# Kernel tuning notes

Hardware: AMD Instinct MI355X
Metric: run time of the kernel (lower is better)

Reference implementation:

```python
import jax, jax.numpy as jnp
import numpy as np

B, N, M, D = 4, 256, 256, 524
EPS = 1e-8


def setup_inputs() -> dict:
    key = jax.random.key(0)
    ks = jax.random.split(key, 16)

    def lin(k, fin, fout):
        kw, kb = jax.random.split(k)
        w = jax.random.normal(kw, (fin, fout), jnp.float32) * (1.0 / np.sqrt(fin))
        b = jax.random.normal(kb, (fout,), jnp.float32) * 0.01
        return w, b

    cw1, cb1 = lin(ks[3], D, 256)
    cw2, cb2 = lin(ks[4], 256, 128)
    cw3, cb3 = lin(ks[5], 128, 1)
    ow1, ob1 = lin(ks[6], D, 128)
    ow2, ob2 = lin(ks[7], 128, 1)
    return {
        "L_bat": jax.random.normal(ks[0], (B, N, M, D), jnp.float32),
        "src_centroids": jax.random.normal(ks[1], (B, N, 3), jnp.float32),
        "tgt_centroids": jax.random.normal(ks[2], (B, M, 3), jnp.float32),
        "cw1": cw1, "cb1": cb1, "cw2": cw2, "cb2": cb2, "cw3": cw3, "cb3": cb3,
        "ow1": ow1, "ob1": ob1, "ow2": ow2, "ob2": ob2,
    }


def _rot_mat_to_quat(R):
    # Shepperd's method, fully batched, scalar-last [x, y, z, w].
    tr = R[:, 0, 0] + R[:, 1, 1] + R[:, 2, 2]
    s0 = jnp.sqrt(jnp.maximum(tr + 1.0, 1e-10)) * 2
    q0 = jnp.stack([(R[:, 2, 1] - R[:, 1, 2]) / s0, (R[:, 0, 2] - R[:, 2, 0]) / s0,
                    (R[:, 1, 0] - R[:, 0, 1]) / s0, 0.25 * s0], axis=-1)
    s1 = jnp.sqrt(jnp.maximum(1.0 + R[:, 0, 0] - R[:, 1, 1] - R[:, 2, 2], 1e-10)) * 2
    q1 = jnp.stack([0.25 * s1, (R[:, 0, 1] + R[:, 1, 0]) / s1,
                    (R[:, 0, 2] + R[:, 2, 0]) / s1, (R[:, 2, 1] - R[:, 1, 2]) / s1], axis=-1)
    s2 = jnp.sqrt(jnp.maximum(1.0 + R[:, 1, 1] - R[:, 0, 0] - R[:, 2, 2], 1e-10)) * 2
    q2 = jnp.stack([(R[:, 0, 1] + R[:, 1, 0]) / s2, 0.25 * s2,
                    (R[:, 1, 2] + R[:, 2, 1]) / s2, (R[:, 0, 2] - R[:, 2, 0]) / s2], axis=-1)
    s3 = jnp.sqrt(jnp.maximum(1.0 + R[:, 2, 2] - R[:, 0, 0] - R[:, 1, 1], 1e-10)) * 2
    q3 = jnp.stack([(R[:, 0, 2] + R[:, 2, 0]) / s3, (R[:, 1, 2] + R[:, 2, 1]) / s3,
                    0.25 * s3, (R[:, 1, 0] - R[:, 0, 1]) / s3], axis=-1)
    c1 = (tr > 0)[:, None]
    c2 = ((R[:, 0, 0] > R[:, 1, 1]) & (R[:, 0, 0] > R[:, 2, 2]))[:, None]
    c3 = (R[:, 1, 1] > R[:, 2, 2])[:, None]
    q = jnp.where(c1, q0, jnp.where(c2, q1, jnp.where(c3, q2, q3)))
    return q / jnp.maximum(jnp.linalg.norm(q, axis=-1, keepdims=True), 1e-12)


def _forward(L_bat, src_centroids, tgt_centroids,
             cw1, cb1, cw2, cb2, cw3, cb3, ow1, ob1, ow2, ob2):
    # corr MLP: [B,N,M,D] -> [B,N,M]
    h = jax.nn.relu(L_bat @ cw1 + cb1)
    h = jax.nn.relu(h @ cw2 + cb2)
    corr_scores = (h @ cw3 + cb3)[..., 0]
    corr_weights = jax.nn.softmax(corr_scores, axis=2)              # softmax over M
    matched = jnp.einsum('bnmd,bnm->bnd', L_bat, corr_weights)      # [B,N,D]
    overlap = jax.nn.sigmoid(jax.nn.relu(matched @ ow1 + ob1) @ ow2 + ob2)  # [B,N,1]
    tgt_matched = jnp.einsum('bnm,bmc->bnc', corr_weights, tgt_centroids)   # [B,N,3]
    w = overlap[..., 0]
    w_norm = w / jnp.maximum(w.sum(axis=1, keepdims=True), EPS)
    src_bar = jnp.einsum('bn,bnc->bc', w_norm, src_centroids)
    tgt_bar = jnp.einsum('bn,bnc->bc', w_norm, tgt_matched)
    src_c = src_centroids - src_bar[:, None, :]
    tgt_c = tgt_matched - tgt_bar[:, None, :]
    H = jnp.einsum('bnc,bn,bnd->bcd', src_c, w_norm, tgt_c)          # [B,3,3]
    U, S, Vh = jnp.linalg.svd(H)
    R_raw = jnp.einsum('bki,bjk->bij', Vh, U)                        # Vh^T @ U^T
    det_sign = jnp.sign(jnp.linalg.det(R_raw))
    corr_fix = jnp.stack([jnp.ones_like(det_sign), jnp.ones_like(det_sign), det_sign], axis=-1)
    Vh_fix = Vh * corr_fix[:, :, None]
    R = jnp.einsum('bki,bjk->bij', Vh_fix, U)
    translation = tgt_bar - jnp.einsum('bij,bj->bi', R, src_bar)
    quaternion = _rot_mat_to_quat(R)
    return quaternion, translation, R, corr_weights, overlap


def reference(L_bat, src_centroids, tgt_centroids,
              cw1, cb1, cw2, cb2, cw3, cb3, ow1, ob1, ow2, ob2):
    return _forward(L_bat, src_centroids, tgt_centroids,
                    cw1, cb1, cw2, cb2, cw3, cb3, ow1, ob1, ow2, ob2)
```

## Files before the change

### kernel.cpp

```cpp
#include <hip/hip_runtime.h>
#include <hip/hip_bf16.h>


#define D_ 524
#define CW_OFF 64
#define OV_OFF 262208

typedef __attribute__((ext_vector_type(8))) short short8;
typedef __attribute__((ext_vector_type(4))) float floatx4;

__device__ __forceinline__ short f2bf(float v) {
  unsigned u = __builtin_bit_cast(unsigned, v);
  unsigned r = (u + 0x7FFFu + ((u >> 16) & 1u)) >> 16;
  return (short)(unsigned short)r;
}
__device__ __forceinline__ float bf2f(short s) {
  unsigned u = ((unsigned)(unsigned short)s) << 16;
  return __builtin_bit_cast(float, u);
}

__global__ void prep_kernel(const float* __restrict__ cw1, const float* __restrict__ cw2,
                            short* __restrict__ w1h, short* __restrict__ w1l,
                            short* __restrict__ w2h, short* __restrict__ w2l) {
  int t = blockIdx.x * 256 + threadIdx.x;
  if (t < 17408) {
    int lane = t & 63, ct = (t >> 6) & 15, kk = t >> 10;
    int col = ct * 16 + (lane & 15);
    int kbase = kk * 32 + ((lane >> 4) << 3);
#pragma unroll
    for (int i = 0; i < 8; ++i) {
      int k = kbase + i;
      float v = (k < D_) ? cw1[k * 256 + col] : 0.f;
      short h = f2bf(v);
      w1h[t * 8 + i] = h;
      w1l[t * 8 + i] = f2bf(v - bf2f(h));
    }
  } else if (t < 21504) {
    int u = t - 17408;
    int lane = u & 63, ct = (u >> 6) & 7, kk = u >> 9;
    int col = ct * 16 + (lane & 15);
    int kbase = kk * 32 + ((lane >> 4) << 3);
#pragma unroll
    for (int i = 0; i < 8; ++i) {
      int k = kbase + i;
      float v = cw2[k * 128 + col];
      short h = f2bf(v);
      w2h[u * 8 + i] = h;
      w2l[u * 8 + i] = f2bf(v - bf2f(h));
    }
  }
}

__global__ __launch_bounds__(256, 2) void main_kernel(
    const float* __restrict__ L, const float* __restrict__ tgt,
    const float* __restrict__ cb1, const float* __restrict__ cb2,
    const float* __restrict__ cw3, const float* __restrict__ cb3,
    const float* __restrict__ ow1, const float* __restrict__ ob1,
    const float* __restrict__ ow2, const float* __restrict__ ob2,
    const short8* __restrict__ w1h, const short8* __restrict__ w1l,
    const short8* __restrict__ w2h, const short8* __restrict__ w2l,
    float* __restrict__ out, float* __restrict__ tgtm) {
  int bn = blockIdx.x;
  int b = bn >> 8;
  int t = threadIdx.x;
  int w = t >> 6, lane = t & 63, l15 = lane & 15, q = lane >> 4;

  __shared__ __attribute__((aligned(16))) short Ah[2][64 * 40];
  __shared__ __attribute__((aligned(16))) short h1s[64 * 264];
  __shared__ float p_all[256];
  __shared__ float redw[256];
  __shared__ float m_s[524];
  __shared__ float o1s[128];
  __shared__ float sS;

  const float* Lbn = L + (size_t)bn * (256 * D_);
  float mac0 = 0.f, mac1 = 0.f, mac2 = 0.f;

  int srow = t >> 2, sko = (t & 3) * 8;

#pragma unroll 1
  for (int mt = 0; mt < 4; ++mt) {
    int m0 = mt * 64;
    const float* Lrow = Lbn + (size_t)(m0 + srow) * D_;

    floatx4 acc[4][4];
#pragma unroll
    for (int r = 0; r < 4; ++r)
#pragma unroll
      for (int c = 0; c < 4; ++c) acc[r][c] = (floatx4)(0.f);

    {
      floatx4 v0 = *(const floatx4*)(Lrow + sko);
      floatx4 v1 = *(const floatx4*)(Lrow + sko + 4);
      short8 sv;
#pragma unroll
      for (int j = 0; j < 4; ++j) { sv[j] = f2bf(v0[j]); sv[4 + j] = f2bf(v1[j]); }
      *(short8*)&Ah[0][srow * 40 + sko] = sv;
    }
    __syncthreads();

#pragma unroll 1
    for (int kk = 0; kk < 17; ++kk) {
      int cb = kk & 1;
      floatx4 nv0, nv1;
      if (kk < 15) {
        nv0 = *(const floatx4*)(Lrow + (kk + 1) * 32 + sko);
        nv1 = *(const floatx4*)(Lrow + (kk + 1) * 32 + sko + 4);
      } else if (kk == 15) {
#pragma unroll
        for (int j = 0; j < 4; ++j) {
          int k0 = 512 + sko + j, k1 = 512 + sko + 4 + j;
          nv0[j] = (k0 < D_) ? Lrow[k0] : 0.f;
          nv1[j] = (k1 < D_) ? Lrow[k1] : 0.f;
        }
      }
      short8 bh[4], bl[4];
#pragma unroll
      for (int c = 0; c < 4; ++c) {
        int f = (kk * 16 + (w * 4 + c)) * 64 + lane;
        bh[c] = w1h[f];
        bl[c] = w1l[f];
      }
      short8 af[4];
#pragma unroll
      for (int r = 0; r < 4; ++r)
        af[r] = *(const short8*)&Ah[cb][(r * 16 + l15) * 40 + q * 8];
#pragma unroll
      for (int r = 0; r < 4; ++r)
#pragma unroll
        for (int c = 0; c < 4; ++c) {
          acc[r][c] = __builtin_amdgcn_mfma_f32_16x16x32_bf16(af[r], bh[c], acc[r][c], 0, 0, 0);
          acc[r][c] = __builtin_amdgcn_mfma_f32_16x16x32_bf16(af[r], bl[c], acc[r][c], 0, 0, 0);
        }
      if (kk < 16) {
        short8 sv;
#pragma unroll
        for (int j = 0; j < 4; ++j) { sv[j] = f2bf(nv0[j]); sv[4 + j] = f2bf(nv1[j]); }
        *(short8*)&Ah[cb ^ 1][srow * 40 + sko] = sv;
      }
      __syncthreads();
    }

#pragma unroll
    for (int c = 0; c < 4; ++c) {
      int col = (w * 4 + c) * 16 + l15;
      float b1 = cb1[col];
#pragma unroll
      for (int r = 0; r < 4; ++r)
#pragma unroll
        for (int i = 0; i < 4; ++i) {
          int row = r * 16 + q * 4 + i;
          h1s[row * 264 + col] = f2bf(fmaxf(acc[r][c][i] + b1, 0.f));
        }
    }
    __syncthreads();

    floatx4 ac2[4][2];
#pragma unroll
    for (int r = 0; r < 4; ++r)
#pragma unroll
      for (int c = 0; c < 2; ++c) ac2[r][c] = (floatx4)(0.f);
#pragma unroll 1
    for (int kk = 0; kk < 8; ++kk) {
      short8 a2[4];
#pragma unroll
      for (int r = 0; r < 4; ++r)
        a2[r] = *(const short8*)&h1s[(r * 16 + l15) * 264 + kk * 32 + q * 8];
      short8 b2h_[2], b2l_[2];
#pragma unroll
      for (int c = 0; c < 2; ++c) {
        int f = (kk * 8 + (w * 2 + c)) * 64 + lane;
        b2h_[c] = w2h[f];
        b2l_[c] = w2l[f];
      }
#pragma unroll
      for (int r = 0; r < 4; ++r)
#pragma unroll
        for (int c = 0; c < 2; ++c) {
          ac2[r][c] = __builtin_amdgcn_mfma_f32_16x16x32_bf16(a2[r], b2h_[c], ac2[r][c], 0, 0, 0);
          ac2[r][c] = __builtin_amdgcn_mfma_f32_16x16x32_bf16(a2[r], b2l_[c], ac2[r][c], 0, 0, 0);
        }
    }

    float pr[4][4];
#pragma unroll
    for (int r = 0; r < 4; ++r)
#pragma unroll
      for (int i = 0; i < 4; ++i) pr[r][i] = 0.f;
#pragma unroll
    for (int c = 0; c < 2; ++c) {
      int col = (w * 2 + c) * 16 + l15;
      float b2 = cb2[col], w3 = cw3[col];
#pragma unroll
      for (int r = 0; r < 4; ++r)
#pragma unroll
        for (int i = 0; i < 4; ++i)
          pr[r][i] += fmaxf(ac2[r][c][i] + b2, 0.f) * w3;
    }
#pragma unroll
    for (int m = 1; m <= 8; m <<= 1)
#pragma unroll
      for (int r = 0; r < 4; ++r)
#pragma unroll
        for (int i = 0; i < 4; ++i) pr[r][i] += __shfl_xor(pr[r][i], m, 64);
    if (l15 == 0) {
#pragma unroll
      for (int r = 0; r < 4; ++r)
#pragma unroll
        for (int i = 0; i < 4; ++i) redw[w * 64 + r * 16 + q * 4 + i] = pr[r][i];
    }
    __syncthreads();
    if (t < 64) {
      float s = redw[t] + redw[64 + t] + redw[128 + t] + redw[192 + t] + cb3[0];
      p_all[m0 + t] = expf(s);
    }
    __syncthreads();

#pragma unroll 4
    for (int m = 0; m < 64; ++m) {
      float pm = p_all[m0 + m];
      const float* Lr = Lbn + (size_t)(m0 + m) * D_;
      mac0 += pm * Lr[t];
      mac1 += pm * Lr[t + 256];
      if (t < 12) mac2 += pm * Lr[t + 512];
    }
  }

  if (t < 64) redw[t] = p_all[t] + p_all[t + 64] + p_all[t + 128] + p_all[t + 192];
  __syncthreads();
  if (t == 0) {
    float s = 0.f;
    for (int i = 0; i < 64; ++i) s += redw[i];
    sS = 1.f / s;
  }
  __syncthreads();
  float invS = sS;
  out[CW_OFF + bn * 256 + t] = p_all[t] * invS;
  m_s[t] = mac0 * invS;
  m_s[t + 256] = mac1 * invS;
  if (t < 12) m_s[t + 512] = mac2 * invS;
  __syncthreads();

  if (t < 128) {
    float a = ob1[t];
#pragma unroll 4
    for (int d = 0; d < D_; ++d) a += m_s[d] * ow1[d * 128 + t];
    o1s[t] = fmaxf(a, 0.f) * ow2[t];
  }
  if (t < 96) {
    int c = t % 3, g = t / 3;
    float s = 0.f;
#pragma unroll
    for (int m = 0; m < 8; ++m) s += p_all[g * 8 + m] * tgt[((b * 256) + g * 8 + m) * 3 + c];
    redw[t] = s;
  }
  __syncthreads();
  if (t == 0) {
    float a = ob2[0];
    for (int j = 0; j < 128; ++j) a += o1s[j];
    out[OV_OFF + bn] = 1.f / (1.f + expf(-a));
  }
  if (t < 3) {
    float s = 0.f;
    for (int g = 0; g < 32; ++g) s += redw[g * 3 + t];
    tgtm[bn * 3 + t] = s * invS;
  }
}

__global__ __launch_bounds__(256) void finalize_kernel(const float* __restrict__ src,
                                                       const float* __restrict__ tgtm,
                                                       float* __restrict__ out) {
  int b = blockIdx.x, t = threadIdx.x;
  __shared__ float red[256];

  auto bsum = [&](float v) -> float {
    red[t] = v;
    __syncthreads();
    for (int s = 128; s > 0; s >>= 1) {
      if (t < s) red[t] += red[t + s];
      __syncthreads();
    }
    float r = red[0];
    __syncthreads();
    return r;
  };

  float wv = out[OV_OFF + b * 256 + t];
  float Sw = bsum(wv);
  float wn = wv / fmaxf(Sw, 1e-8f);
  float sc[3], tm[3];
#pragma unroll
  for (int c = 0; c < 3; ++c) {
    sc[c] = src[(b * 256 + t) * 3 + c];
    tm[c] = tgtm[(b * 256 + t) * 3 + c];
  }
  float sb[3], tb[3];
#pragma unroll
  for (int c = 0; c < 3; ++c) sb[c] = bsum(wn * sc[c]);
#pragma unroll
  for (int c = 0; c < 3; ++c) tb[c] = bsum(wn * tm[c]);
  float Hv[9];
#pragma unroll
  for (int c = 0; c < 3; ++c)
#pragma unroll
    for (int d = 0; d < 3; ++d)
      Hv[c * 3 + d] = bsum((sc[c] - sb[c]) * wn * (tm[d] - tb[d]));

  if (t == 0) {
    double H[3][3];
    for (int i = 0; i < 3; ++i)
      for (int j = 0; j < 3; ++j) H[i][j] = (double)Hv[i * 3 + j];
    double A[3][3], V[3][3] = {{1, 0, 0}, {0, 1, 0}, {0, 0, 1}};
    for (int i = 0; i < 3; ++i)
      for (int j = 0; j < 3; ++j) {
        double s = 0;
        for (int k = 0; k < 3; ++k) s += H[k][i] * H[k][j];
        A[i][j] = s;
      }
    const int PQ[3][2] = {{0, 1}, {0, 2}, {1, 2}};
    for (int sweep = 0; sweep < 30; ++sweep)
      for (int r = 0; r < 3; ++r) {
        int p = PQ[r][0], qq = PQ[r][1];
        double apq = A[p][qq];
        if (fabs(apq) < 1e-300) continue;
        double tau = (A[qq][qq] - A[p][p]) / (2.0 * apq);
        double tt = (tau >= 0 ? 1.0 : -1.0) / (fabs(tau) + sqrt(1.0 + tau * tau));
        double cc = 1.0 / sqrt(1.0 + tt * tt), ss = tt * cc;
        for (int k = 0; k < 3; ++k) {
          double akp = A[k][p], akq = A[k][qq];
          A[k][p] = cc * akp - ss * akq;
          A[k][qq] = ss * akp + cc * akq;
        }
        for (int k = 0; k < 3; ++k) {
          double apk = A[p][k], aqk = A[qq][k];
          A[p][k] = cc * apk - ss * aqk;
          A[qq][k] = ss * apk + cc * aqk;
        }
        for (int k = 0; k < 3; ++k) {
          double vkp = V[k][p], vkq = V[k][qq];
          V[k][p] = cc * vkp - ss * vkq;
          V[k][qq] = ss * vkp + cc * vkq;
        }
      }
    int idx[3] = {0, 1, 2};
    for (int i = 0; i < 2; ++i)
      for (int j = i + 1; j < 3; ++j)
        if (A[idx[j]][idx[j]] > A[idx[i]][idx[i]]) { int tmp = idx[i]; idx[i] = idx[j]; idx[j] = tmp; }
    double v0[3], v1[3], v2[3];
    for (int k = 0; k < 3; ++k) {
      v0[k] = V[k][idx[0]];
      v1[k] = V[k][idx[1]];
      v2[k] = V[k][idx[2]];
    }
    double u0[3], u1[3], u2[3];
    for (int j = 0; j < 3; ++j) {
      u0[j] = H[j][0] * v0[0] + H[j][1] * v0[1] + H[j][2] * v0[2];
      u1[j] = H[j][0] * v1[0] + H[j][1] * v1[1] + H[j][2] * v1[2];
    }
    double n0 = sqrt(u0[0] * u0[0] + u0[1] * u0[1] + u0[2] * u0[2]);
    n0 = (n0 > 1e-300) ? n0 : 1e-300;
    for (int j = 0; j < 3; ++j) u0[j] /= n0;
    double d01 = u0[0] * u1[0] + u0[1] * u1[1] + u0[2] * u1[2];
    for (int j = 0; j < 3; ++j) u1[j] -= d01 * u0[j];
    double n1 = sqrt(u1[0] * u1[0] + u1[1] * u1[1] + u1[2] * u1[2]);
    n1 = (n1 > 1e-300) ? n1 : 1e-300;
    for (int j = 0; j < 3; ++j) u1[j] /= n1;
    u2[0] = u0[1] * u1[2] - u0[2] * u1[1];
    u2[1] = u0[2] * u1[0] - u0[0] * u1[2];
    u2[2] = u0[0] * u1[1] - u0[1] * u1[0];
    double Rr[3][3];
    for (int i = 0; i < 3; ++i)
      for (int j = 0; j < 3; ++j)
        Rr[i][j] = v0[i] * u0[j] + v1[i] * u1[j] + v2[i] * u2[j];
    double det = Rr[0][0] * (Rr[1][1] * Rr[2][2] - Rr[1][2] * Rr[2][1]) -
                 Rr[0][1] * (Rr[1][0] * Rr[2][2] - Rr[1][2] * Rr[2][0]) +
                 Rr[0][2] * (Rr[1][0] * Rr[2][1] - Rr[1][1] * Rr[2][0]);
    double sg = (det >= 0) ? 1.0 : -1.0;
    double R[3][3];
    for (int i = 0; i < 3; ++i)
      for (int j = 0; j < 3; ++j)
        R[i][j] = v0[i] * u0[j] + v1[i] * u1[j] + sg * v2[i] * u2[j];
    double trv[3];
    for (int i = 0; i < 3; ++i)
      trv[i] = (double)tb[i] - (R[i][0] * sb[0] + R[i][1] * sb[1] + R[i][2] * sb[2]);
    double qv[4];
    double tr = R[0][0] + R[1][1] + R[2][2];
    if (tr > 0) {
      double S = sqrt(fmax(tr + 1.0, 1e-10)) * 2.0;
      qv[0] = (R[2][1] - R[1][2]) / S;
      qv[1] = (R[0][2] - R[2][0]) / S;
      qv[2] = (R[1][0] - R[0][1]) / S;
      qv[3] = 0.25 * S;
    } else if (R[0][0] > R[1][1] && R[0][0] > R[2][2]) {
      double S = sqrt(fmax(1.0 + R[0][0] - R[1][1] - R[2][2], 1e-10)) * 2.0;
      qv[0] = 0.25 * S;
      qv[1] = (R[0][1] + R[1][0]) / S;
      qv[2] = (R[0][2] + R[2][0]) / S;
      qv[3] = (R[2][1] - R[1][2]) / S;
    } else if (R[1][1] > R[2][2]) {
      double S = sqrt(fmax(1.0 + R[1][1] - R[0][0] - R[2][2], 1e-10)) * 2.0;
      qv[0] = (R[0][1] + R[1][0]) / S;
      qv[1] = 0.25 * S;
      qv[2] = (R[1][2] + R[2][1]) / S;
      qv[3] = (R[0][2] - R[2][0]) / S;
    } else {
      double S = sqrt(fmax(1.0 + R[2][2] - R[0][0] - R[1][1], 1e-10)) * 2.0;
      qv[0] = (R[0][2] + R[2][0]) / S;
      qv[1] = (R[1][2] + R[2][1]) / S;
      qv[2] = 0.25 * S;
      qv[3] = (R[1][0] - R[0][1]) / S;
    }
    double qn = sqrt(qv[0] * qv[0] + qv[1] * qv[1] + qv[2] * qv[2] + qv[3] * qv[3]);
    qn = fmax(qn, 1e-12);
    for (int k = 0; k < 4; ++k) out[b * 4 + k] = (float)(qv[k] / qn);
    for (int i = 0; i < 3; ++i) out[16 + b * 3 + i] = (float)trv[i];
    for (int i = 0; i < 3; ++i)
      for (int j = 0; j < 3; ++j) out[28 + b * 9 + i * 3 + j] = (float)R[i][j];
  }
}

extern "C" void kernel_launch(void* const* d_in, const int* in_sizes, int n_in,
                              void* d_out, int out_size, void* d_ws, size_t ws_size,
                              hipStream_t stream) {
  const float* L = (const float*)d_in[0];
  const float* src = (const float*)d_in[1];
  const float* tgt = (const float*)d_in[2];
  const float* cw1 = (const float*)d_in[3];
  const float* cb1 = (const float*)d_in[4];
  const float* cw2 = (const float*)d_in[5];
  const float* cb2 = (const float*)d_in[6];
  const float* cw3 = (const float*)d_in[7];
  const float* cb3 = (const float*)d_in[8];
  const float* ow1 = (const float*)d_in[9];
  const float* ob1 = (const float*)d_in[10];
  const float* ow2 = (const float*)d_in[11];
  const float* ob2 = (const float*)d_in[12];
  float* out = (float*)d_out;

  char* ws = (char*)d_ws;
  short* w1h = (short*)(ws);
  short* w1l = (short*)(ws + 278528);
  short* w2h = (short*)(ws + 557056);
  short* w2l = (short*)(ws + 622592);
  float* tgtm = (float*)(ws + 688128);

  hipLaunchKernelGGL(prep_kernel, dim3(84), dim3(256), 0, stream, cw1, cw2, w1h, w1l, w2h, w2l);
  hipLaunchKernelGGL(main_kernel, dim3(1024), dim3(256), 0, stream,
                     L, tgt, cb1, cb2, cw3, cb3, ow1, ob1, ow2, ob2,
                     (const short8*)w1h, (const short8*)w1l,
                     (const short8*)w2h, (const short8*)w2l, out, tgtm);
  hipLaunchKernelGGL(finalize_kernel, dim3(4), dim3(256), 0, stream, src, tgtm, out);
}
```

Before: 1.140 ms.

## Fold overlap MLP first layer into GEMM via linearity, widen block to 512 threads

Uses linearity to replace the weighted sum of L rows followed by the ow1 matvec with an extra GEMM column block (ow1 appended to cw1 in bf16 hi only), accumulated per row and then weighted by p. This removes the second full pass over L from global memory for the weighted mean. The block doubles to 512 threads processing two 64-row tiles per k-step, and the padding of the second-layer buffer changes. The change adds MFMA work and drops precision on the ow1 path to single bf16, which risks accuracy.

```diff
diff --git a/kernel.cpp b/kernel.cpp
--- a/kernel.cpp
+++ b/kernel.cpp
@@ -5,6 +5,12 @@
 #define D_ 524
 #define CW_OFF 64
 #define OV_OFF 262208
+
+#define W1H_OFF 0
+#define W1L_OFF 417792
+#define W2H_OFF 696320
+#define W2L_OFF 761856
+#define TGTM_OFF 827392
 
 typedef __attribute__((ext_vector_type(8))) short short8;
 typedef __attribute__((ext_vector_type(4))) float floatx4;
@@ -19,31 +25,32 @@
   return __builtin_bit_cast(float, u);
 }
 
-__global__ void prep_kernel(const float* __restrict__ cw1, const float* __restrict__ cw2,
+__global__ void prep_kernel(const float* __restrict__ cw1, const float* __restrict__ ow1,
+                            const float* __restrict__ cw2,
                             short* __restrict__ w1h, short* __restrict__ w1l,
                             short* __restrict__ w2h, short* __restrict__ w2l) {
   int t = blockIdx.x * 256 + threadIdx.x;
-  if (t < 17408) {
-    int lane = t & 63, ct = (t >> 6) & 15, kk = t >> 10;
-    int col = ct * 16 + (lane & 15);
-    int kbase = kk * 32 + ((lane >> 4) << 3);
+  if (t < 26112) {
+    int lane = t & 63, ct = (t >> 6) % 24, kk = t / 1536;
+    int cl = lane & 15, kb = kk * 32 + ((lane >> 4) << 3);
+    bool isW1 = ct < 16;
+    int lo_base = ((kk * 16 + ct) * 64 + lane) * 8;
 #pragma unroll
     for (int i = 0; i < 8; ++i) {
-      int k = kbase + i;
-      float v = (k < D_) ? cw1[k * 256 + col] : 0.f;
+      int k = kb + i;
+      float v = 0.f;
+      if (k < D_) v = isW1 ? cw1[k * 256 + ct * 16 + cl] : ow1[k * 128 + (ct - 16) * 16 + cl];
       short h = f2bf(v);
       w1h[t * 8 + i] = h;
-      w1l[t * 8 + i] = f2bf(v - bf2f(h));
-    }
-  } else if (t < 21504) {
-    int u = t - 17408;
+      if (isW1) w1l[lo_base + i] = f2bf(v - bf2f(h));
+    }
+  } else if (t < 30208) {
+    int u = t - 26112;
     int lane = u & 63, ct = (u >> 6) & 7, kk = u >> 9;
-    int col = ct * 16 + (lane & 15);
-    int kbase = kk * 32 + ((lane >> 4) << 3);
+    int col = ct * 16 + (lane & 15), kb = kk * 32 + ((lane >> 4) << 3);
 #pragma unroll
     for (int i = 0; i < 8; ++i) {
-      int k = kbase + i;
-      float v = cw2[k * 128 + col];
+      float v = cw2[(kb + i) * 128 + col];
       short h = f2bf(v);
       w2h[u * 8 + i] = h;
       w2l[u * 8 + i] = f2bf(v - bf2f(h));
@@ -51,51 +58,51 @@
   }
 }
 
-__global__ __launch_bounds__(256, 2) void main_kernel(
+__global__ __launch_bounds__(512, 2) void main_kernel(
     const float* __restrict__ L, const float* __restrict__ tgt,
     const float* __restrict__ cb1, const float* __restrict__ cb2,
     const float* __restrict__ cw3, const float* __restrict__ cb3,
-    const float* __restrict__ ow1, const float* __restrict__ ob1,
-    const float* __restrict__ ow2, const float* __restrict__ ob2,
+    const float* __restrict__ ob1, const float* __restrict__ ow2,
+    const float* __restrict__ ob2,
     const short8* __restrict__ w1h, const short8* __restrict__ w1l,
     const short8* __restrict__ w2h, const short8* __restrict__ w2l,
     float* __restrict__ out, float* __restrict__ tgtm) {
-  int bn = blockIdx.x;
-  int b = bn >> 8;
-  int t = threadIdx.x;
+  int bn = blockIdx.x, b = bn >> 8, t = threadIdx.x;
   int w = t >> 6, lane = t & 63, l15 = lane & 15, q = lane >> 4;
 
-  __shared__ __attribute__((aligned(16))) short Ah[2][64 * 40];
-  __shared__ __attribute__((aligned(16))) short h1s[64 * 264];
+  __shared__ __attribute__((aligned(16))) short Ah[2][2][64 * 40];
+  __shared__ __attribute__((aligned(16))) short h1s[64 * 272];
   __shared__ float p_all[256];
-  __shared__ float redw[256];
-  __shared__ float m_s[524];
-  __shared__ float o1s[128];
+  __shared__ float redw[512];
   __shared__ float sS;
 
   const float* Lbn = L + (size_t)bn * (256 * D_);
-  float mac0 = 0.f, mac1 = 0.f, mac2 = 0.f;
-
-  int srow = t >> 2, sko = (t & 3) * 8;
+  float ua = 0.f;
+
+  int mt_s = t >> 8, srow = (t >> 2) & 63, sko = (t & 3) * 8;
 
 #pragma unroll 1
-  for (int mt = 0; mt < 4; ++mt) {
-    int m0 = mt * 64;
-    const float* Lrow = Lbn + (size_t)(m0 + srow) * D_;
-
-    floatx4 acc[4][4];
-#pragma unroll
-    for (int r = 0; r < 4; ++r)
-#pragma unroll
-      for (int c = 0; c < 4; ++c) acc[r][c] = (floatx4)(0.f);
+  for (int mp = 0; mp < 2; ++mp) {
+    const float* Lr0 = Lbn + (size_t)(mp * 128 + mt_s * 64 + srow) * D_;
+
+    floatx4 acc[2][4][2];
+    floatx4 accg[2][4];
+#pragma unroll
+    for (int mt = 0; mt < 2; ++mt)
+#pragma unroll
+      for (int r = 0; r < 4; ++r) {
+        acc[mt][r][0] = (floatx4)(0.f);
+        acc[mt][r][1] = (floatx4)(0.f);
+        accg[mt][r] = (floatx4)(0.f);
+      }
 
     {
-      floatx4 v0 = *(const floatx4*)(Lrow + sko);
-      floatx4 v1 = *(const floatx4*)(Lrow + sko + 4);
+      floatx4 v0 = *(const floatx4*)(Lr0 + sko);
+      floatx4 v1 = *(const floatx4*)(Lr0 + sko + 4);
       short8 sv;
 #pragma unroll
       for (int j = 0; j < 4; ++j) { sv[j] = f2bf(v0[j]); sv[4 + j] = f2bf(v1[j]); }
-      *(short8*)&Ah[0][srow * 40 + sko] = sv;
+      *(short8*)&Ah[0][mt_s][srow * 40 + sko] = sv;
     }
     __syncthreads();
 
@@ -104,125 +111,115 @@
       int cb = kk & 1;
       floatx4 nv0, nv1;
       if (kk < 15) {
-        nv0 = *(const floatx4*)(Lrow + (kk + 1) * 32 + sko);
-        nv1 = *(const floatx4*)(Lrow + (kk + 1) * 32 + sko + 4);
+        nv0 = *(const floatx4*)(Lr0 + (kk + 1) * 32 + sko);
+        nv1 = *(const floatx4*)(Lr0 + (kk + 1) * 32 + sko + 4);
       } else if (kk == 15) {
 #pragma unroll
         for (int j = 0; j < 4; ++j) {
-          int k0 = 512 + sko + j, k1 = 512 + sko + 4 + j;
-          nv0[j] = (k0 < D_) ? Lrow[k0] : 0.f;
-          nv1[j] = (k1 < D_) ? Lrow[k1] : 0.f;
-        }
-      }
-      short8 bh[4], bl[4];
-#pragma unroll
-      for (int c = 0; c < 4; ++c) {
-        int f = (kk * 16 + (w * 4 + c)) * 64 + lane;
-        bh[c] = w1h[f];
-        bl[c] = w1l[f];
-      }
-      short8 af[4];
-#pragma unroll
-      for (int r = 0; r < 4; ++r)
-        af[r] = *(const short8*)&Ah[cb][(r * 16 + l15) * 40 + q * 8];
-#pragma unroll
-      for (int r = 0; r < 4; ++r)
-#pragma unroll
-        for (int c = 0; c < 4; ++c) {
-          acc[r][c] = __builtin_amdgcn_mfma_f32_16x16x32_bf16(af[r], bh[c], acc[r][c], 0, 0, 0);
-          acc[r][c] = __builtin_amdgcn_mfma_f32_16x16x32_bf16(af[r], bl[c], acc[r][c], 0, 0, 0);
+          int k0 = 512 + sko + j, k1 = 516 + sko + j;
+          nv0[j] = (k0 < D_) ? Lr0[k0] : 0.f;
+          nv1[j] = (k1 < D_) ? Lr0[k1] : 0.f;
+        }
+      }
+      short8 bh0 = w1h[(kk * 24 + 2 * w) * 64 + lane];
+      short8 bh1 = w1h[(kk * 24 + 2 * w + 1) * 64 + lane];
+      short8 gh = w1h[(kk * 24 + 16 + w) * 64 + lane];
+      short8 bl0 = w1l[(kk * 16 + 2 * w) * 64 + lane];
+      short8 bl1 = w1l[(kk * 16 + 2 * w + 1) * 64 + lane];
+      short8 af[2][4];
+#pragma unroll
+      for (int mt = 0; mt < 2; ++mt)
+#pragma unroll
+        for (int r = 0; r < 4; ++r)
+          af[mt][r] = *(const short8*)&Ah[cb][mt][(r * 16 + l15) * 40 + q * 8];
+#pragma unroll
+      for (int mt = 0; mt < 2; ++mt)
+#pragma unroll
+        for (int r = 0; r < 4; ++r) {
+          acc[mt][r][0] = __builtin_amdgcn_mfma_f32_16x16x32_bf16(af[mt][r], bh0, acc[mt][r][0], 0, 0, 0);
+          acc[mt][r][0] = __builtin_amdgcn_mfma_f32_16x16x32_bf16(af[mt][r], bl0, acc[mt][r][0], 0, 0, 0);
+          acc[mt][r][1] = __builtin_amdgcn_mfma_f32_16x16x32_bf16(af[mt][r], bh1, acc[mt][r][1], 0, 0, 0);
+          acc[mt][r][1] = __builtin_amdgcn_mfma_f32_16x16x32_bf16(af[mt][r], bl1, acc[mt][r][1], 0, 0, 0);
+          accg[mt][r] = __builtin_amdgcn_mfma_f32_16x16x32_bf16(af[mt][r], gh, accg[mt][r], 0, 0, 0);
         }
       if (kk < 16) {
         short8 sv;
 #pragma unroll
         for (int j = 0; j < 4; ++j) { sv[j] = f2bf(nv0[j]); sv[4 + j] = f2bf(nv1[j]); }
-        *(short8*)&Ah[cb ^ 1][srow * 40 + sko] = sv;
+        *(short8*)&Ah[cb ^ 1][mt_s][srow * 40 + sko] = sv;
       }
       __syncthreads();
     }
 
-#pragma unroll
-    for (int c = 0; c < 4; ++c) {
-      int col = (w * 4 + c) * 16 + l15;
-      float b1 = cb1[col];
+#pragma unroll 1
+    for (int mt = 0; mt < 2; ++mt) {
+      int m0 = mp * 128 + mt * 64;
+#pragma unroll
+      for (int c = 0; c < 2; ++c) {
+        int col = (2 * w + c) * 16 + l15;
+        float b1 = cb1[col];
+#pragma unroll
+        for (int r = 0; r < 4; ++r)
+#pragma unroll
+          for (int i = 0; i < 4; ++i)
+            h1s[(r * 16 + q * 4 + i) * 272 + col] = f2bf(fmaxf(acc[mt][r][c][i] + b1, 0.f));
+      }
+      __syncthreads();
+
+      floatx4 ac2[4];
+#pragma unroll
+      for (int r = 0; r < 4; ++r) ac2[r] = (floatx4)(0.f);
+#pragma unroll 1
+      for (int kk = 0; kk < 8; ++kk) {
+        short8 b2h_ = w2h[(kk * 8 + w) * 64 + lane];
+        short8 b2l_ = w2l[(kk * 8 + w) * 64 + lane];
+        short8 a2[4];
+#pragma unroll
+        for (int r = 0; r < 4; ++r)
+          a2[r] = *(const short8*)&h1s[(r * 16 + l15) * 272 + kk * 32 + q * 8];
+#pragma unroll
+        for (int r = 0; r < 4; ++r) {
+          ac2[r] = __builtin_amdgcn_mfma_f32_16x16x32_bf16(a2[r], b2h_, ac2[r], 0, 0, 0);
+          ac2[r] = __builtin_amdgcn_mfma_f32_16x16x32_bf16(a2[r], b2l_, ac2[r], 0, 0, 0);
+        }
+      }
+      int col2 = w * 16 + l15;
+      float b2 = cb2[col2], w3 = cw3[col2];
+      float pr[4][4];
 #pragma unroll
       for (int r = 0; r < 4; ++r)
 #pragma unroll
-        for (int i = 0; i < 4; ++i) {
-          int row = r * 16 + q * 4 + i;
-          h1s[row * 264 + col] = f2bf(fmaxf(acc[r][c][i] + b1, 0.f));
-        }
-    }
-    __syncthreads();
-
-    floatx4 ac2[4][2];
-#pragma unroll
-    for (int r = 0; r < 4; ++r)
-#pragma unroll
-      for (int c = 0; c < 2; ++c) ac2[r][c] = (floatx4)(0.f);
-#pragma unroll 1
-    for (int kk = 0; kk < 8; ++kk) {
-      short8 a2[4];
+        for (int i = 0; i < 4; ++i)
+          pr[r][i] = fmaxf(ac2[r][i] + b2, 0.f) * w3;
+#pragma unroll
+      for (int m = 1; m <= 8; m <<= 1)
+#pragma unroll
+        for (int r = 0; r < 4; ++r)
+#pragma unroll
+          for (int i = 0; i < 4; ++i) pr[r][i] += __shfl_xor(pr[r][i], m, 64);
+      if (l15 == 0) {
+#pragma unroll
+        for (int r = 0; r < 4; ++r)
+#pragma unroll
+          for (int i = 0; i < 4; ++i) redw[w * 64 + r * 16 + q * 4 + i] = pr[r][i];
+      }
+      __syncthreads();
+      if (t < 64) {
+        float s = cb3[0];
+#pragma unroll
+        for (int ww = 0; ww < 8; ++ww) s += redw[ww * 64 + t];
+        p_all[m0 + t] = expf(s);
+      }
+      __syncthreads();
+      float gv = 0.f;
 #pragma unroll
       for (int r = 0; r < 4; ++r)
-        a2[r] = *(const short8*)&h1s[(r * 16 + l15) * 264 + kk * 32 + q * 8];
-      short8 b2h_[2], b2l_[2];
-#pragma unroll
-      for (int c = 0; c < 2; ++c) {
-        int f = (kk * 8 + (w * 2 + c)) * 64 + lane;
-        b2h_[c] = w2h[f];
-        b2l_[c] = w2l[f];
-      }
-#pragma unroll
-      for (int r = 0; r < 4; ++r)
-#pragma unroll
-        for (int c = 0; c < 2; ++c) {
-          ac2[r][c] = __builtin_amdgcn_mfma_f32_16x16x32_bf16(a2[r], b2h_[c], ac2[r][c], 0, 0, 0);
-          ac2[r][c] = __builtin_amdgcn_mfma_f32_16x16x32_bf16(a2[r], b2l_[c], ac2[r][c], 0, 0, 0);
-        }
-    }
-
-    float pr[4][4];
-#pragma unroll
-    for (int r = 0; r < 4; ++r)
-#pragma unroll
-      for (int i = 0; i < 4; ++i) pr[r][i] = 0.f;
-#pragma unroll
-    for (int c = 0; c < 2; ++c) {
-      int col = (w * 2 + c) * 16 + l15;
-      float b2 = cb2[col], w3 = cw3[col];
-#pragma unroll
-      for (int r = 0; r < 4; ++r)
 #pragma unroll
         for (int i = 0; i < 4; ++i)
-          pr[r][i] += fmaxf(ac2[r][c][i] + b2, 0.f) * w3;
-    }
-#pragma unroll
-    for (int m = 1; m <= 8; m <<= 1)
-#pragma unroll
-      for (int r = 0; r < 4; ++r)
-#pragma unroll
-        for (int i = 0; i < 4; ++i) pr[r][i] += __shfl_xor(pr[r][i], m, 64);
-    if (l15 == 0) {
-#pragma unroll
-      for (int r = 0; r < 4; ++r)
-#pragma unroll
-        for (int i = 0; i < 4; ++i) redw[w * 64 + r * 16 + q * 4 + i] = pr[r][i];
-    }
-    __syncthreads();
-    if (t < 64) {
-      float s = redw[t] + redw[64 + t] + redw[128 + t] + redw[192 + t] + cb3[0];
-      p_all[m0 + t] = expf(s);
-    }
-    __syncthreads();
-
-#pragma unroll 4
-    for (int m = 0; m < 64; ++m) {
-      float pm = p_all[m0 + m];
-      const float* Lr = Lbn + (size_t)(m0 + m) * D_;
-      mac0 += pm * Lr[t];
-      mac1 += pm * Lr[t + 256];
-      if (t < 12) mac2 += pm * Lr[t + 512];
+          gv += p_all[m0 + r * 16 + q * 4 + i] * accg[mt][r][i];
+      gv += __shfl_xor(gv, 16, 64);
+      gv += __shfl_xor(gv, 32, 64);
+      ua += gv;
     }
   }
 
@@ -235,34 +232,32 @@
   }
   __syncthreads();
   float invS = sS;
-  out[CW_OFF + bn * 256 + t] = p_all[t] * invS;
-  m_s[t] = mac0 * invS;
-  m_s[t + 256] = mac1 * invS;
-  if (t < 12) m_s[t + 512] = mac2 * invS;
-  __syncthreads();
-
-  if (t < 128) {
-    float a = ob1[t];
-#pragma unroll 4
-    for (int d = 0; d < D_; ++d) a += m_s[d] * ow1[d * 128 + t];
-    o1s[t] = fmaxf(a, 0.f) * ow2[t];
+  if (t < 256) out[CW_OFF + bn * 256 + t] = p_all[t] * invS;
+
+  {
+    float u = ua * invS + ob1[w * 16 + l15];
+    float r = fmaxf(u, 0.f) * ow2[w * 16 + l15];
+    if (q != 0) r = 0.f;
+#pragma unroll
+    for (int m = 1; m <= 32; m <<= 1) r += __shfl_xor(r, m, 64);
+    if (lane == 0) redw[256 + w] = r;
   }
   if (t < 96) {
     int c = t % 3, g = t / 3;
     float s = 0.f;
 #pragma unroll
     for (int m = 0; m < 8; ++m) s += p_all[g * 8 + m] * tgt[((b * 256) + g * 8 + m) * 3 + c];
-    redw[t] = s;
+    redw[320 + t] = s;
   }
   __syncthreads();
   if (t == 0) {
-    float a = ob2[0];
-    for (int j = 0; j < 128; ++j) a += o1s[j];
-    out[OV_OFF + bn] = 1.f / (1.f + expf(-a));
+    float o = ob2[0];
+    for (int ww = 0; ww < 8; ++ww) o += redw[256 + ww];
+    out[OV_OFF + bn] = 1.f / (1.f + expf(-o));
   }
   if (t < 3) {
     float s = 0.f;
-    for (int g = 0; g < 32; ++g) s += redw[g * 3 + t];
+    for (int g = 0; g < 32; ++g) s += redw[320 + g * 3 + t];
     tgtm[bn * 3 + t] = s * invS;
   }
 }
@@ -438,15 +433,15 @@
   float* out = (float*)d_out;
 
   char* ws = (char*)d_ws;
-  short* w1h = (short*)(ws);
-  short* w1l = (short*)(ws + 278528);
-  short* w2h = (short*)(ws + 557056);
-  short* w2l = (short*)(ws + 622592);
-  float* tgtm = (float*)(ws + 688128);
-
-  hipLaunchKernelGGL(prep_kernel, dim3(84), dim3(256), 0, stream, cw1, cw2, w1h, w1l, w2h, w2l);
-  hipLaunchKernelGGL(main_kernel, dim3(1024), dim3(256), 0, stream,
-                     L, tgt, cb1, cb2, cw3, cb3, ow1, ob1, ow2, ob2,
+  short* w1h = (short*)(ws + W1H_OFF);
+  short* w1l = (short*)(ws + W1L_OFF);
+  short* w2h = (short*)(ws + W2H_OFF);
+  short* w2l = (short*)(ws + W2L_OFF);
+  float* tgtm = (float*)(ws + TGTM_OFF);
+
+  hipLaunchKernelGGL(prep_kernel, dim3(118), dim3(256), 0, stream, cw1, ow1, cw2, w1h, w1l, w2h, w2l);
+  hipLaunchKernelGGL(main_kernel, dim3(1024), dim3(512), 0, stream,
+                     L, tgt, cb1, cb2, cw3, cb3, ob1, ow2, ob2,
                      (const short8*)w1h, (const short8*)w1l,
                      (const short8*)w2h, (const short8*)w2l, out, tgtm);
   hipLaunchKernelGGL(finalize_kernel, dim3(4), dim3(256), 0, stream, src, tgtm, out);
```

Measured after the change: 2.180 ms. 1.91x slower.
